# Optimization experiments

Hardware: AMD Instinct MI355X
Metric: run time of the kernel (lower is better)

Reference implementation:

```python
import jax, jax.numpy as jnp
import numpy as np
import math

IMAGE_SIZE = 512
N_ANGLES = 180
BATCH = 4


def _shepp_logan_filter(size):
    # Matches _get_fourier_filter(size, 'shepp-logan') in the torch module.
    n = np.concatenate([np.arange(1, size // 2 + 1, 2), np.arange(size // 2 - 1, 0, -2)])
    f = np.zeros(size, dtype=np.float64)
    f[0] = 0.25
    f[1::2] = -1.0 / (np.pi * n) ** 2
    ff = 2.0 * np.real(np.fft.fft(f))
    omega = np.pi * np.fft.fftfreq(size)[1:]
    ff[1:] *= np.sin(omega) / omega
    return jnp.asarray(ff, dtype=jnp.float32)


def setup_inputs() -> dict:
    key = jax.random.key(0)
    sinogram = jax.random.normal(key, (BATCH, N_ANGLES, IMAGE_SIZE), dtype=jnp.float32)
    return {"sinogram": sinogram}


def _inverse_radon(sinogram):
    B, A, P = sinogram.shape
    S = P  # image_size == proj_size (required by the torch filter expand)
    # --- FFT ramp filtering (pad_size == P for power-of-two P >= 64, so pad_width = 0) ---
    ff = _shepp_logan_filter(P)  # [P]
    filtered = jnp.real(
        jnp.fft.ifft(jnp.fft.fft(sinogram, axis=-1) * ff, axis=-1)
    ).astype(sinogram.dtype)  # [B, A, P]

    # --- backprojection grid (note: x axis is reversed, as in the torch meshgrid) ---
    x = jnp.arange(S - 1, -1, -1, dtype=jnp.float32) - S // 2  # [W]
    y = jnp.arange(S, dtype=jnp.float32) - S // 2              # [H]
    angles_rad = jnp.linspace(0.0, 180.0, A) * (math.pi / 180.0)  # [A]
    half = P // 2

    def body(acc, inp):
        theta, row = inp  # theta scalar, row: [B, P] filtered projection for this angle
        # unnormalized sample position; equals grid_sample(align_corners=True) coord
        p = x[None, :] * jnp.sin(theta) + y[:, None] * jnp.cos(theta) + half  # [H, W]
        i0f = jnp.floor(p)
        frac = p - i0f  # [H, W]
        i0 = i0f.astype(jnp.int32)
        i1 = i0 + 1

        def tap(idx):
            # bilinear tap with zeros padding (out-of-range taps contribute 0)
            valid = (idx >= 0) & (idx <= P - 1)  # [H, W]
            v = jnp.take(row, jnp.clip(idx, 0, P - 1), axis=1)  # [B, H, W]
            return jnp.where(valid[None], v, jnp.zeros((), dtype=row.dtype))

        contrib = (1.0 - frac)[None] * tap(i0) + frac[None] * tap(i1)  # [B, H, W]
        return acc + contrib, None

    out0 = jnp.zeros((B, S, S), dtype=sinogram.dtype)
    out, _ = jax.lax.scan(body, out0, (angles_rad, jnp.swapaxes(filtered, 0, 1)))
    out = out * (math.pi / (2.0 * A))

    # circle mask
    radius = S // 2
    mask = (x[None, :] ** 2 + y[:, None] ** 2) <= radius ** 2  # [H, W]
    out = out * mask[None].astype(out.dtype)
    return out[:, None]  # [B, 1, S, S]


def reference(sinogram):
    return _inverse_radon(sinogram)
```

## Files before the change

### kernel.cpp

```cpp
#include <hip/hip_runtime.h>
#include <math.h>

#define P      512
#define NA     180
#define NB     4
#define FOFF4  64
#define FS4    (FOFF4 + 4 * P + FOFF4)
#define GUARD  512
#define TS     16
#define WPOS   28
#define WSF4   (WPOS * 4)
#define ASEG   60
#define NTILES (32 * 32)

#if __has_builtin(__builtin_amdgcn_fractf)
#define FRACT(x) __builtin_amdgcn_fractf(x)
#else
#define FRACT(x) ((x) - floorf(x))
#endif

typedef float f4 __attribute__((ext_vector_type(4), aligned(16)));

constexpr double PI_D = 3.14159265358979323846264338327950288;

struct D512 { double v[512]; };
struct F512 { float v[512]; };
struct SCT2 { float sc[NA][2]; };

constexpr double cosap(double x) {
    double invf[13] = {};
    double f = 1.0; invf[0] = 1.0;
    for (int n = 1; n <= 12; ++n) { f *= (double)((2 * n - 1) * (2 * n)); invf[n] = 1.0 / f; }
    const double x2 = x * x;
    double r = invf[12];
    for (int n = 11; n >= 0; --n) r = invf[n] - x2 * r;
    return r;
}
constexpr double sinap(double x) {
    double invf[13] = {};
    double f = 1.0; invf[0] = 1.0;
    for (int n = 1; n <= 12; ++n) { f *= (double)((2 * n) * (2 * n + 1)); invf[n] = 1.0 / f; }
    const double x2 = x * x;
    double r = invf[12];
    for (int n = 11; n >= 0; --n) r = invf[n] - x2 * r;
    return x * r;
}

constexpr D512 make_ct() {
    D512 t{};
    for (int ph = 0; ph < 512; ++ph) {
        const int q = ph >> 7, r = ph & 127;
        double v = 0.0;
        if (q == 0)      v =  cosap(PI_D * (double)r / 256.0);
        else if (q == 1) v = -cosap(PI_D * (double)(128 - r) / 256.0);
        else if (q == 2) v = -cosap(PI_D * (double)r / 256.0);
        else             v =  cosap(PI_D * (double)(128 - r) / 256.0);
        t.v[ph] = v;
    }
    return t;
}
constexpr D512 CT = make_ct();

constexpr F512 make_ffg() {
    F512 t{};
    double fv[128] = {};
    for (int mm = 0; mm < 128; ++mm) {
        const double pn = PI_D * (double)(2 * mm + 1);
        fv[mm] = -1.0 / (pn * pn);
    }
    for (int o = 0; o <= 256; ++o) {
        double s = 0.0;
        for (int mm = 0; mm < 128; ++mm)
            s += fv[mm] * CT.v[(o * (2 * mm + 1)) & 511];
        double ff = 0.5 + 4.0 * s;
        if (o > 0) {
            const double w = PI_D * (double)o / 512.0;
            ff *= sinap(w) / w;
        }
        t.v[o] = (float)ff;
    }
    for (int o = 257; o < 512; ++o) t.v[o] = t.v[512 - o];
    return t;
}
constexpr F512 FFG = make_ffg();

constexpr F512 make_hr_part(int lo, int hi) {
    F512 t{};
    for (int o = lo; o < hi; ++o) {
        double s2 = 0.0;
        for (int k = 1; k < 256; ++k)
            s2 += (double)FFG.v[k] * CT.v[(o * k) & 511];
        double s = (double)FFG.v[0] + (double)FFG.v[256] * CT.v[(o * 256) & 511] + 2.0 * s2;
        t.v[o] = (float)(s / 512.0);
    }
    return t;
}
constexpr F512 HR_A = make_hr_part(0, 129);
constexpr F512 HR_B = make_hr_part(129, 257);

constexpr F512 make_hr() {
    F512 t{};
    for (int o = 0; o < 129; ++o)   t.v[o] = HR_A.v[o];
    for (int o = 129; o < 257; ++o) t.v[o] = HR_B.v[o];
    for (int o = 257; o < 512; ++o) t.v[o] = t.v[512 - o];
    return t;
}
__constant__ F512 HRC = make_hr();

constexpr SCT2 make_sct() {
    SCT2 t{};
    for (int a = 0; a < NA; ++a) {
        const float thf = (float)a * (float)(PI_D / 179.0);
        const double x = (double)thf;
        double sv, cv;
        if (x <= PI_D * 0.5) { sv = sinap(x);        cv =  cosap(x); }
        else                 { sv = sinap(PI_D - x); cv = -cosap(PI_D - x); }
        t.sc[a][0] = (float)sv;
        t.sc[a][1] = (float)cv;
    }
    return t;
}
__constant__ SCT2 SCT = make_sct();

__global__ __launch_bounds__(512) void ir_filter(const float* __restrict__ sino,
                                                 float* __restrict__ fil2,
                                                 float* __restrict__ qbt) {
    __shared__ __align__(16) float row2[4][2 * P];
    __shared__ __align__(16) float sOut[4 * P];
    const int a = blockIdx.x;
    const int t = threadIdx.x;

    const int b = t >> 7;
    const int tt = t & 127;

    const float* src = sino + ((size_t)b * NA + a) * P;
    const float4 v = *(const float4*)(src + 4 * tt);
    *(float4*)&row2[b][4 * tt] = v;
    *(float4*)&row2[b][4 * tt + P] = v;
    __syncthreads();

    const int base0 = P + 4 * tt;
    float4 A = *(const float4*)&row2[b][base0];
    float a0 = 0.f, a1 = 0.f, a2 = 0.f, a3 = 0.f;
    #pragma unroll 4
    for (int J = 0; J < P; J += 4) {
        const float4 Bv = *(const float4*)&row2[b][base0 - J - 4];
        const float h0 = HRC.v[J], h1 = HRC.v[J + 1], h2v = HRC.v[J + 2], h3 = HRC.v[J + 3];
        a0 = fmaf(h0, A.x, a0); a0 = fmaf(h1, Bv.w, a0); a0 = fmaf(h2v, Bv.z, a0); a0 = fmaf(h3, Bv.y, a0);
        a1 = fmaf(h0, A.y, a1); a1 = fmaf(h1, A.x, a1); a1 = fmaf(h2v, Bv.w, a1); a1 = fmaf(h3, Bv.z, a1);
        a2 = fmaf(h0, A.z, a2); a2 = fmaf(h1, A.y, a2); a2 = fmaf(h2v, A.x, a2); a2 = fmaf(h3, Bv.w, a2);
        a3 = fmaf(h0, A.w, a3); a3 = fmaf(h1, A.z, a3); a3 = fmaf(h2v, A.y, a3); a3 = fmaf(h3, A.x, a3);
        A = Bv;
    }
    const int o0 = 16 * tt + b;
    sOut[o0]      = a0;
    sOut[o0 + 4]  = a1;
    sOut[o0 + 8]  = a2;
    sOut[o0 + 12] = a3;
    __syncthreads();

    float* frow = fil2 + (size_t)a * FS4;
    *(f4*)(frow + FOFF4 + 4 * t) = *(const f4*)(sOut + 4 * t);
    if (t < FOFF4) {
        frow[t] = 0.f;
        frow[FOFF4 + 4 * P + t] = 0.f;
    }

    const float sa = SCT.sc[a][0];
    const float ca = SCT.sc[a][1];
    #pragma unroll
    for (int i = 0; i < 2; ++i) {
        const int tile = t + 512 * i;
        const int bx = tile & 31, by = tile >> 5;
        const float xlo = (float)(240 - 16 * bx);
        const float ylo = (float)(16 * by - 256);
        const float yhi = (float)(16 * by - 241);
        const float pmin = fmaf(sa, xlo, fminf(ca * ylo, ca * yhi) + 256.0f);
        const int base = ((int)floorf(pmin) - 2) & ~1;
        qbt[tile * NA + a] = (float)(256 - base);
    }
}

__global__ __launch_bounds__(256) void ir_backproject(const float* __restrict__ fil2,
                                                      const float* __restrict__ qbt,
                                                      float* __restrict__ out) {
    __shared__ __align__(16) float win[ASEG * WSF4 + 16];

    const int t = threadIdx.x;
    const int w0 = blockIdx.x * TS, h0 = blockIdx.y * TS;
    const float* qrow = qbt + (blockIdx.y * 32 + blockIdx.x) * NA;

    const int w = w0 + (t & 15);
    const int h = h0 + (t >> 4);

    const int ix = 255 - w;
    const int iy = h - 256;
    const int m = (ix * ix + iy * iy) <= 256 * 256;

    float* o0 = out + (size_t)h * P + w;

    if (__syncthreads_count(m) == 0) {
        o0[0] = 0.f;
        o0[P * P] = 0.f;
        o0[2 * P * P] = 0.f;
        o0[3 * P * P] = 0.f;
        return;
    }

    const float xf = (float)ix;
    const float yf = (float)iy;
    float acc0 = 0.f, acc1 = 0.f, acc2 = 0.f, acc3 = 0.f;

    #pragma unroll
    for (int seg = 0; seg < 3; ++seg) {
        const int A0 = seg * ASEG;

        for (int idx = t; idx < ASEG * WPOS; idx += 256) {
            const int al = idx / WPOS;
            const int i = idx - al * WPOS;
            const int a = A0 + al;
            const int base = 256 - (int)qrow[a];
            const int off = a * FS4 + FOFF4 + 4 * (base + i);
            const f4 vv = *(const f4*)(fil2 + off);
            *(f4*)(win + al * WSF4 + 4 * i) = vv;
        }
        __syncthreads();

        #pragma unroll 4
        for (int al = 0; al < ASEG; ++al) {
            const float ss = SCT.sc[A0 + al][0];
            const float cc = SCT.sc[A0 + al][1];
            const float qb = qrow[A0 + al];
            const float q = fmaf(xf, ss, fmaf(yf, cc, qb));
            const int j = (int)q;
            const float fr = FRACT(q);
            const float omf = 1.f - fr;
            const f4 W0 = *(const f4*)(win + al * WSF4 + 4 * j);
            const f4 W1 = *(const f4*)(win + al * WSF4 + 4 * j + 4);
            acc0 = fmaf(omf, W0.x, fmaf(fr, W1.x, acc0));
            acc1 = fmaf(omf, W0.y, fmaf(fr, W1.y, acc1));
            acc2 = fmaf(omf, W0.z, fmaf(fr, W1.z, acc2));
            acc3 = fmaf(omf, W0.w, fmaf(fr, W1.w, acc3));
        }
        if (seg < 2) __syncthreads();
    }

    const float scale = (float)(M_PI / (2.0 * NA));
    o0[0]         = m ? acc0 * scale : 0.f;
    o0[P * P]     = m ? acc1 * scale : 0.f;
    o0[2 * P * P] = m ? acc2 * scale : 0.f;
    o0[3 * P * P] = m ? acc3 * scale : 0.f;
}

extern "C" void kernel_launch(void* const* d_in, const int* in_sizes, int n_in,
                              void* d_out, int out_size, void* d_ws, size_t ws_size,
                              hipStream_t stream) {
    const float* sino = (const float*)d_in[0];
    float* out = (float*)d_out;
    float* ws = (float*)d_ws;

    float* qbt   = ws;
    float* fil2  = ws + NTILES * NA + GUARD;

    ir_filter<<<NA, 512, 0, stream>>>(sino, fil2, qbt);

    dim3 gridB(P / TS, P / TS, 1);
    ir_backproject<<<gridB, 256, 0, stream>>>(fil2, qbt, out);
}
```

Measured before the change: 97.39 us.

## Compute two vertically adjacent pixels per thread sharing window loads

Each thread now handles two rows of the tile (128 threads per block). For the two pixels it loads three consecutive window entries once and picks which pair each pixel uses, relying on their projection indices differing by at most one when cos is small in magnitude. The sign of cos sets which pixel is the base, hence the per-segment angle ranges, with plain per-pixel handling near 0 and 180 degrees. This removes LDS loads and repeated per-angle setup in exchange for more registers, fewer threads to stage the window, and a hard-coded split of angle ranges.

```diff
diff --git a/kernel.cpp b/kernel.cpp
--- a/kernel.cpp
+++ b/kernel.cpp
@@ -20,6 +20,13 @@
 #endif
 
 typedef float f4 __attribute__((ext_vector_type(4), aligned(16)));
+
+static __device__ __forceinline__ f4 fma4(float s, f4 b, f4 c) {
+    f4 r;
+    r.x = fmaf(s, b.x, c.x); r.y = fmaf(s, b.y, c.y);
+    r.z = fmaf(s, b.z, c.z); r.w = fmaf(s, b.w, c.w);
+    return r;
+}
 
 constexpr double PI_D = 3.14159265358979323846264338327950288;
 
@@ -181,7 +188,45 @@
     }
 }
 
-__global__ __launch_bounds__(256) void ir_backproject(const float* __restrict__ fil2,
+__device__ __forceinline__ void ang_plain(const float* wr, float xf, float yf,
+                                          float ss, float cc, float qb, f4& acc) {
+    const float q = fmaf(xf, ss, fmaf(yf, cc, qb));
+    const int j = (int)q;
+    const float fr = FRACT(q);
+    const f4 W0 = *(const f4*)(wr + 4 * j);
+    const f4 W1 = *(const f4*)(wr + 4 * j + 4);
+    acc = fma4(1.f - fr, W0, fma4(fr, W1, acc));
+}
+
+template <bool CPOS>
+__device__ __forceinline__ void ang_shared(const float* wr, float xf, float yf0, float yf1,
+                                           float ss, float cc, float qb,
+                                           f4& accT, f4& accB) {
+    const float q0 = fmaf(xf, ss, fmaf(yf0, cc, qb));
+    const float q1 = fmaf(xf, ss, fmaf(yf1, cc, qb));
+    const int j0 = (int)q0, j1 = (int)q1;
+    const float fr0 = FRACT(q0), fr1 = FRACT(q1);
+    const float of0 = 1.f - fr0, of1 = 1.f - fr1;
+    const int jm = CPOS ? j0 : j1;
+    const f4 R0 = *(const f4*)(wr + 4 * jm);
+    const f4 R1 = *(const f4*)(wr + 4 * jm + 4);
+    const f4 R2 = *(const f4*)(wr + 4 * jm + 8);
+    if (CPOS) {
+        const bool d = (j1 != j0);
+        const f4 X0 = d ? R1 : R0;
+        const f4 X1 = d ? R2 : R1;
+        accT = fma4(of0, R0, fma4(fr0, R1, accT));
+        accB = fma4(of1, X0, fma4(fr1, X1, accB));
+    } else {
+        const bool d = (j0 != j1);
+        const f4 X0 = d ? R1 : R0;
+        const f4 X1 = d ? R2 : R1;
+        accT = fma4(of0, X0, fma4(fr0, X1, accT));
+        accB = fma4(of1, R0, fma4(fr1, R1, accB));
+    }
+}
+
+__global__ __launch_bounds__(128) void ir_backproject(const float* __restrict__ fil2,
                                                       const float* __restrict__ qbt,
                                                       float* __restrict__ out) {
     __shared__ __align__(16) float win[ASEG * WSF4 + 16];
@@ -191,31 +236,37 @@
     const float* qrow = qbt + (blockIdx.y * 32 + blockIdx.x) * NA;
 
     const int w = w0 + (t & 15);
-    const int h = h0 + (t >> 4);
+    const int r = t >> 4;
+    const int h = h0 + 2 * r;
 
     const int ix = 255 - w;
-    const int iy = h - 256;
-    const int m = (ix * ix + iy * iy) <= 256 * 256;
+    const int iy0 = h - 256;
+    const int iy1 = iy0 + 1;
+    const int m0 = (ix * ix + iy0 * iy0) <= 256 * 256;
+    const int m1 = (ix * ix + iy1 * iy1) <= 256 * 256;
 
     float* o0 = out + (size_t)h * P + w;
 
-    if (__syncthreads_count(m) == 0) {
-        o0[0] = 0.f;
-        o0[P * P] = 0.f;
-        o0[2 * P * P] = 0.f;
-        o0[3 * P * P] = 0.f;
+    if (__syncthreads_count(m0 | m1) == 0) {
+        #pragma unroll
+        for (int b = 0; b < 4; ++b) {
+            o0[(size_t)b * P * P]     = 0.f;
+            o0[(size_t)b * P * P + P] = 0.f;
+        }
         return;
     }
 
     const float xf = (float)ix;
-    const float yf = (float)iy;
-    float acc0 = 0.f, acc1 = 0.f, acc2 = 0.f, acc3 = 0.f;
+    const float yf0 = (float)iy0;
+    const float yf1 = (float)iy1;
+    f4 accT = {0.f, 0.f, 0.f, 0.f};
+    f4 accB = {0.f, 0.f, 0.f, 0.f};
 
     #pragma unroll
     for (int seg = 0; seg < 3; ++seg) {
         const int A0 = seg * ASEG;
 
-        for (int idx = t; idx < ASEG * WPOS; idx += 256) {
+        for (int idx = t; idx < ASEG * WPOS; idx += 128) {
             const int al = idx / WPOS;
             const int i = idx - al * WPOS;
             const int a = A0 + al;
@@ -226,30 +277,66 @@
         }
         __syncthreads();
 
-        #pragma unroll 4
-        for (int al = 0; al < ASEG; ++al) {
-            const float ss = SCT.sc[A0 + al][0];
-            const float cc = SCT.sc[A0 + al][1];
-            const float qb = qrow[A0 + al];
-            const float q = fmaf(xf, ss, fmaf(yf, cc, qb));
-            const int j = (int)q;
-            const float fr = FRACT(q);
-            const float omf = 1.f - fr;
-            const f4 W0 = *(const f4*)(win + al * WSF4 + 4 * j);
-            const f4 W1 = *(const f4*)(win + al * WSF4 + 4 * j + 4);
-            acc0 = fmaf(omf, W0.x, fmaf(fr, W1.x, acc0));
-            acc1 = fmaf(omf, W0.y, fmaf(fr, W1.y, acc1));
-            acc2 = fmaf(omf, W0.z, fmaf(fr, W1.z, acc2));
-            acc3 = fmaf(omf, W0.w, fmaf(fr, W1.w, acc3));
+        if (seg == 0) {
+            #pragma unroll
+            for (int al = 0; al < 3; ++al) {
+                const float ss = SCT.sc[al][0], cc = SCT.sc[al][1];
+                const float qb = qrow[al];
+                const float* wr = win + al * WSF4;
+                ang_plain(wr, xf, yf0, ss, cc, qb, accT);
+                ang_plain(wr, xf, yf1, ss, cc, qb, accB);
+            }
+            #pragma unroll 2
+            for (int al = 3; al < 60; ++al) {
+                const float ss = SCT.sc[al][0], cc = SCT.sc[al][1];
+                const float qb = qrow[al];
+                ang_shared<true>(win + al * WSF4, xf, yf0, yf1, ss, cc, qb, accT, accB);
+            }
+        } else if (seg == 1) {
+            #pragma unroll 2
+            for (int al = 0; al < 30; ++al) {
+                const int a = 60 + al;
+                const float ss = SCT.sc[a][0], cc = SCT.sc[a][1];
+                const float qb = qrow[a];
+                ang_shared<true>(win + al * WSF4, xf, yf0, yf1, ss, cc, qb, accT, accB);
+            }
+            #pragma unroll 2
+            for (int al = 30; al < 60; ++al) {
+                const int a = 60 + al;
+                const float ss = SCT.sc[a][0], cc = SCT.sc[a][1];
+                const float qb = qrow[a];
+                ang_shared<false>(win + al * WSF4, xf, yf0, yf1, ss, cc, qb, accT, accB);
+            }
+        } else {
+            #pragma unroll 2
+            for (int al = 0; al < 57; ++al) {
+                const int a = 120 + al;
+                const float ss = SCT.sc[a][0], cc = SCT.sc[a][1];
+                const float qb = qrow[a];
+                ang_shared<false>(win + al * WSF4, xf, yf0, yf1, ss, cc, qb, accT, accB);
+            }
+            #pragma unroll
+            for (int al = 57; al < 60; ++al) {
+                const int a = 120 + al;
+                const float ss = SCT.sc[a][0], cc = SCT.sc[a][1];
+                const float qb = qrow[a];
+                const float* wr = win + al * WSF4;
+                ang_plain(wr, xf, yf0, ss, cc, qb, accT);
+                ang_plain(wr, xf, yf1, ss, cc, qb, accB);
+            }
         }
         if (seg < 2) __syncthreads();
     }
 
     const float scale = (float)(M_PI / (2.0 * NA));
-    o0[0]         = m ? acc0 * scale : 0.f;
-    o0[P * P]     = m ? acc1 * scale : 0.f;
-    o0[2 * P * P] = m ? acc2 * scale : 0.f;
-    o0[3 * P * P] = m ? acc3 * scale : 0.f;
+    o0[0]                     = m0 ? accT.x * scale : 0.f;
+    o0[P]                     = m1 ? accB.x * scale : 0.f;
+    o0[(size_t)P * P]         = m0 ? accT.y * scale : 0.f;
+    o0[(size_t)P * P + P]     = m1 ? accB.y * scale : 0.f;
+    o0[(size_t)2 * P * P]     = m0 ? accT.z * scale : 0.f;
+    o0[(size_t)2 * P * P + P] = m1 ? accB.z * scale : 0.f;
+    o0[(size_t)3 * P * P]     = m0 ? accT.w * scale : 0.f;
+    o0[(size_t)3 * P * P + P] = m1 ? accB.w * scale : 0.f;
 }
 
 extern "C" void kernel_launch(void* const* d_in, const int* in_sizes, int n_in,
@@ -265,5 +352,5 @@
     ir_filter<<<NA, 512, 0, stream>>>(sino, fil2, qbt);
 
     dim3 gridB(P / TS, P / TS, 1);
-    ir_backproject<<<gridB, 256, 0, stream>>>(fil2, qbt, out);
-}
+    ir_backproject<<<gridB, 128, 0, stream>>>(fil2, qbt, out);
+}
```

Measured after the change: 119.4 us. 22.6% more time.

## Split angle range across two thread halves per tile with shared-memory reduction

Applied to the files above, without the earlier changes.

Doubles the backprojection block to 512 threads, with each half of the block accumulating a different half of the 180 angles for the same 16x16 pixel tile. The two partial sums are combined through shared memory at the end. Each segment now stages 30 angles for each half, so the window loads per sync keep the same size. This adds thread-level parallelism and latency hiding per tile, at the cost of an extra reduction step and higher per-block resource use.

```diff
diff --git a/kernel.cpp b/kernel.cpp
--- a/kernel.cpp
+++ b/kernel.cpp
@@ -10,7 +10,8 @@
 #define TS     16
 #define WPOS   28
 #define WSF4   (WPOS * 4)
-#define ASEG   60
+#define HSEG   30
+#define NSLOT  (2 * HSEG)
 #define NTILES (32 * 32)
 
 #if __has_builtin(__builtin_amdgcn_fractf)
@@ -181,17 +182,19 @@
     }
 }
 
-__global__ __launch_bounds__(256) void ir_backproject(const float* __restrict__ fil2,
-                                                      const float* __restrict__ qbt,
-                                                      float* __restrict__ out) {
-    __shared__ __align__(16) float win[ASEG * WSF4 + 16];
+__global__ __launch_bounds__(512, 8) void ir_backproject(const float* __restrict__ fil2,
+                                                         const float* __restrict__ qbt,
+                                                         float* __restrict__ out) {
+    __shared__ __align__(16) float win[NSLOT * WSF4];
 
     const int t = threadIdx.x;
+    const int half = t >> 8;
+    const int tl = t & 255;
     const int w0 = blockIdx.x * TS, h0 = blockIdx.y * TS;
     const float* qrow = qbt + (blockIdx.y * 32 + blockIdx.x) * NA;
 
-    const int w = w0 + (t & 15);
-    const int h = h0 + (t >> 4);
+    const int w = w0 + (tl & 15);
+    const int h = h0 + (tl >> 4);
 
     const int ix = 255 - w;
     const int iy = h - 256;
@@ -200,56 +203,67 @@
     float* o0 = out + (size_t)h * P + w;
 
     if (__syncthreads_count(m) == 0) {
-        o0[0] = 0.f;
-        o0[P * P] = 0.f;
-        o0[2 * P * P] = 0.f;
-        o0[3 * P * P] = 0.f;
+        if (t < 256) {
+            o0[0] = 0.f;
+            o0[(size_t)P * P] = 0.f;
+            o0[(size_t)2 * P * P] = 0.f;
+            o0[(size_t)3 * P * P] = 0.f;
+        }
         return;
     }
 
     const float xf = (float)ix;
     const float yf = (float)iy;
-    float acc0 = 0.f, acc1 = 0.f, acc2 = 0.f, acc3 = 0.f;
+    f4 acc = {0.f, 0.f, 0.f, 0.f};
 
     #pragma unroll
     for (int seg = 0; seg < 3; ++seg) {
-        const int A0 = seg * ASEG;
-
-        for (int idx = t; idx < ASEG * WPOS; idx += 256) {
-            const int al = idx / WPOS;
-            const int i = idx - al * WPOS;
-            const int a = A0 + al;
+        const int A0 = seg * HSEG;
+
+        for (int idx = t; idx < NSLOT * WPOS; idx += 512) {
+            const int sl = idx / WPOS;
+            const int i = idx - sl * WPOS;
+            const int a = (sl < HSEG) ? (A0 + sl) : (60 + A0 + sl);
             const int base = 256 - (int)qrow[a];
             const int off = a * FS4 + FOFF4 + 4 * (base + i);
             const f4 vv = *(const f4*)(fil2 + off);
-            *(f4*)(win + al * WSF4 + 4 * i) = vv;
+            *(f4*)(win + sl * WSF4 + 4 * i) = vv;
         }
         __syncthreads();
 
-        #pragma unroll 4
-        for (int al = 0; al < ASEG; ++al) {
-            const float ss = SCT.sc[A0 + al][0];
-            const float cc = SCT.sc[A0 + al][1];
-            const float qb = qrow[A0 + al];
+        const int abase = half * 90 + A0;
+        const int sbase = half * HSEG;
+        #pragma unroll 5
+        for (int al = 0; al < HSEG; ++al) {
+            const int a = abase + al;
+            const float ss = SCT.sc[a][0];
+            const float cc = SCT.sc[a][1];
+            const float qb = qrow[a];
             const float q = fmaf(xf, ss, fmaf(yf, cc, qb));
             const int j = (int)q;
             const float fr = FRACT(q);
             const float omf = 1.f - fr;
-            const f4 W0 = *(const f4*)(win + al * WSF4 + 4 * j);
-            const f4 W1 = *(const f4*)(win + al * WSF4 + 4 * j + 4);
-            acc0 = fmaf(omf, W0.x, fmaf(fr, W1.x, acc0));
-            acc1 = fmaf(omf, W0.y, fmaf(fr, W1.y, acc1));
-            acc2 = fmaf(omf, W0.z, fmaf(fr, W1.z, acc2));
-            acc3 = fmaf(omf, W0.w, fmaf(fr, W1.w, acc3));
-        }
-        if (seg < 2) __syncthreads();
-    }
-
-    const float scale = (float)(M_PI / (2.0 * NA));
-    o0[0]         = m ? acc0 * scale : 0.f;
-    o0[P * P]     = m ? acc1 * scale : 0.f;
-    o0[2 * P * P] = m ? acc2 * scale : 0.f;
-    o0[3 * P * P] = m ? acc3 * scale : 0.f;
+            const float* wr = win + (sbase + al) * WSF4;
+            const f4 W0 = *(const f4*)(wr + 4 * j);
+            const f4 W1 = *(const f4*)(wr + 4 * j + 4);
+            acc.x = fmaf(omf, W0.x, fmaf(fr, W1.x, acc.x));
+            acc.y = fmaf(omf, W0.y, fmaf(fr, W1.y, acc.y));
+            acc.z = fmaf(omf, W0.z, fmaf(fr, W1.z, acc.z));
+            acc.w = fmaf(omf, W0.w, fmaf(fr, W1.w, acc.w));
+        }
+        __syncthreads();
+    }
+
+    if (t >= 256) *(f4*)(win + 4 * tl) = acc;
+    __syncthreads();
+    if (t < 256) {
+        const f4 b = *(const f4*)(win + 4 * tl);
+        const float scale = (float)(M_PI / (2.0 * NA));
+        o0[0]                 = m ? (acc.x + b.x) * scale : 0.f;
+        o0[(size_t)P * P]     = m ? (acc.y + b.y) * scale : 0.f;
+        o0[(size_t)2 * P * P] = m ? (acc.z + b.z) * scale : 0.f;
+        o0[(size_t)3 * P * P] = m ? (acc.w + b.w) * scale : 0.f;
+    }
 }
 
 extern "C" void kernel_launch(void* const* d_in, const int* in_sizes, int n_in,
@@ -265,5 +279,5 @@
     ir_filter<<<NA, 512, 0, stream>>>(sino, fil2, qbt);
 
     dim3 gridB(P / TS, P / TS, 1);
-    ir_backproject<<<gridB, 256, 0, stream>>>(fil2, qbt, out);
-}
+    ir_backproject<<<gridB, 512, 0, stream>>>(fil2, qbt, out);
+}
```

Result: slower. 104.2 us (+7.0%).
